# Kernel tuning notes

Measured on AMD Instinct MI355X. Metric: run time of the kernel, lower is better.

## Reference

```python
import jax, jax.numpy as jnp
import numpy as np

D = 256
H = 4
HD = D // H


def setup_inputs() -> dict:
    key = jax.random.key(0)
    ks = jax.random.split(key, 12)
    A, T = 64, 512
    s = 1.0 / np.sqrt(D)
    return {
        "features": jax.random.normal(ks[0], (A, T, D), jnp.float32),
        "positions": jax.random.normal(ks[1], (A, T, 2), jnp.float32),
        "Wq": jax.random.normal(ks[2], (D, D), jnp.float32) * s,
        "bq": jnp.zeros((D,), jnp.float32),
        "Wk": jax.random.normal(ks[3], (D, D), jnp.float32) * s,
        "bk": jnp.zeros((D,), jnp.float32),
        "Wv": jax.random.normal(ks[4], (D, D), jnp.float32) * s,
        "bv": jnp.zeros((D,), jnp.float32),
        "Wo": jax.random.normal(ks[5], (D, D), jnp.float32) * s,
        "bo": jnp.zeros((D,), jnp.float32),
        "max_distance": 2,
        "time_window": 64,
    }


def _sparse_mask(positions, max_distance, time_window):
    # positions: [A, T, 2] -> allowed [A, T, T]
    A, T, _ = positions.shape
    diff = positions[:, :, None, :] - positions[:, None, :, :]  # [A,T,T,2]
    dist2 = jnp.sum(diff * diff, axis=-1)                       # [A,T,T]
    t = jnp.arange(T)
    tmask = jnp.abs(t[:, None] - t[None, :]) <= time_window      # [T,T]
    return (dist2 <= float(max_distance) ** 2) & tmask[None]     # [A,T,T]


def reference(features, positions, Wq, bq, Wk, bk, Wv, bv, Wo, bo,
              max_distance, time_window):
    A, T, Dm = features.shape
    allowed = _sparse_mask(positions, max_distance, time_window)  # [A,T,T]
    q = features @ Wq.T + bq
    k = features @ Wk.T + bk
    v = features @ Wv.T + bv
    # split heads: [A, T, H, HD]
    q = q.reshape(A, T, H, HD)
    k = k.reshape(A, T, H, HD)
    v = v.reshape(A, T, H, HD)
    scale = 1.0 / np.sqrt(HD)
    scores = jnp.einsum("athd,ashd->ahts", q, k) * scale          # [A,H,T,T]
    scores = jnp.where(allowed[:, None], scores, -jnp.inf)
    attn = jax.nn.softmax(scores, axis=-1)
    out = jnp.einsum("ahts,ashd->athd", attn, v).reshape(A, T, Dm)
    return out @ Wo.T + bo
```

## Files before the change

### kernel.cpp

```cpp
#include <hip/hip_runtime.h>
#include <hip/hip_bf16.h>
#include <cstdint>
#include <cstddef>

typedef __attribute__((ext_vector_type(8))) _Float16 half8;
typedef __attribute__((ext_vector_type(4))) float floatx4;

#define MFMA16(a, b, c) __builtin_amdgcn_mfma_f32_16x16x32_f16((a), (b), (c), 0, 0, 0)

#define GLOAD_LDS16(g, l)                                                     \
    __builtin_amdgcn_global_load_lds(                                         \
        (const __attribute__((address_space(1))) void*)(g),                   \
        (__attribute__((address_space(3))) void*)(l), 16, 0, 0)

#define NFEAT 8388608

__device__ __forceinline__ void stage_dma(
    const _Float16* __restrict__ src, _Float16* __restrict__ lds,
    int wid, int lane)
{
#pragma unroll
    for (int i = 0; i < 4; ++i) {
        int grp = wid * 4 + i;
        int row = grp * 8 + (lane >> 3);
        int sc  = (lane & 7) ^ (row & 7);
        GLOAD_LDS16(src + (size_t)row * 256 + sc * 8, lds + grp * 512);
    }
}

__device__ __forceinline__ void stage_f32_s(
    const float* __restrict__ src, _Float16* __restrict__ lds, int tid,
    int dst_stride)
{
#pragma unroll
    for (int i = 0; i < 4; ++i) {
        int g   = tid + 256 * i;
        int row = g >> 3, chd = g & 7;
        int chs = chd ^ (row & 7);
        const float* s = src + (size_t)row * 256 + chs * 8;
        float4 v0 = *(const float4*)s;
        float4 v1 = *(const float4*)(s + 4);
        half8 h = { (_Float16)v0.x, (_Float16)v0.y, (_Float16)v0.z, (_Float16)v0.w,
                    (_Float16)v1.x, (_Float16)v1.y, (_Float16)v1.z, (_Float16)v1.w };
        *(half8*)(&lds[row * dst_stride + chd * 8]) = h;
    }
}

__global__ __launch_bounds__(256) void qkv_fused(
    const float* __restrict__ feat,
    const float* __restrict__ Wq, const float* __restrict__ Wk,
    const float* __restrict__ Wv,
    const float* __restrict__ bq, const float* __restrict__ bk,
    const float* __restrict__ bv,
    _Float16* __restrict__ Qb, _Float16* __restrict__ Kb, _Float16* __restrict__ Vb)
{
    __shared__ _Float16 Xs[128 * 256];
    __shared__ _Float16 Ws[128 * 64];

    const int n   = blockIdx.x;
    const int idx = n >> 3;
    const int bm  = (n & 7) * 32 + (idx >> 1);
    const int bn  = idx & 1;

    const int tid  = threadIdx.x;
    const int lane = tid & 63, wid = tid >> 6;
    const int quad = lane >> 4, l16 = lane & 15;
    const int wm = wid & 1, wn = wid >> 1;

    const float* Xg = feat + (size_t)bm * 128 * 256;
#pragma unroll
    for (int slab = 0; slab < 4; ++slab)
        stage_f32_s(Xg + slab * 64, Xs + slab * 64, tid, 256);
    __syncthreads();

#pragma unroll 1
    for (int z = 0; z < 3; ++z) {
        const float* W    = (z == 0) ? Wq : (z == 1) ? Wk : Wv;
        const float* bias = (z == 0) ? bq : (z == 1) ? bk : bv;
        _Float16*    outp = (z == 0) ? Qb : (z == 1) ? Kb : Vb;
        const float* Wg = W + (size_t)bn * 128 * 256;

        floatx4 acc[4][4] = {};
#pragma unroll 1
        for (int ks = 0; ks < 4; ++ks) {
            stage_f32_s(Wg + ks * 64, Ws, tid, 64);
            __syncthreads();
#pragma unroll
            for (int kh = 0; kh < 2; ++kh) {
                half8 af[4], bf[4];
#pragma unroll
                for (int mi = 0; mi < 4; ++mi) {
                    int row = wm * 64 + mi * 16 + l16;
                    int cs  = (kh * 4 + quad) ^ (row & 7);
                    af[mi] = *(const half8*)(&Xs[row * 256 + ks * 64 + cs * 8]);
                }
#pragma unroll
                for (int ni = 0; ni < 4; ++ni) {
                    int row = wn * 64 + ni * 16 + l16;
                    int cs  = (kh * 4 + quad) ^ (row & 7);
                    bf[ni] = *(const half8*)(&Ws[row * 64 + cs * 8]);
                }
#pragma unroll
                for (int mi = 0; mi < 4; ++mi)
#pragma unroll
                    for (int ni = 0; ni < 4; ++ni)
                        acc[mi][ni] = MFMA16(af[mi], bf[ni], acc[mi][ni]);
            }
            __syncthreads();
        }

#pragma unroll
        for (int ni = 0; ni < 4; ++ni) {
            int col = bn * 128 + wn * 64 + ni * 16 + l16;
            float bv2 = bias[col];
#pragma unroll
            for (int mi = 0; mi < 4; ++mi)
#pragma unroll
                for (int r = 0; r < 4; ++r) {
                    int row = bm * 128 + wm * 64 + mi * 16 + quad * 4 + r;
                    outp[(size_t)row * 256 + col] = (_Float16)(acc[mi][ni][r] + bv2);
                }
        }
    }
}

__global__ __launch_bounds__(256) void out_gemm(
    const _Float16* __restrict__ attnH, const float* __restrict__ Wo,
    const float* __restrict__ bo, float* __restrict__ out)
{
    __shared__ _Float16 As[128 * 64];
    __shared__ _Float16 Bs[128 * 64];

    const int n   = blockIdx.x;
    const int idx = n >> 3;
    const int bm  = (n & 7) * 32 + (idx >> 1);
    const int bn  = idx & 1;

    const int tid  = threadIdx.x;
    const int lane = tid & 63, wid = tid >> 6;
    const int quad = lane >> 4, l16 = lane & 15;
    const int wm = wid & 1, wn = wid >> 1;

    floatx4 acc[4][4] = {};
    const float* Wg = Wo + (size_t)bn * 128 * 256;

    for (int k0 = 0; k0 < 256; k0 += 64) {
        stage_dma(attnH + (size_t)bm * 128 * 256 + k0, As, wid, lane);
        stage_f32_s(Wg + k0, Bs, tid, 64);
        __syncthreads();
#pragma unroll
        for (int kh = 0; kh < 2; ++kh) {
            half8 af[4], bf[4];
#pragma unroll
            for (int mi = 0; mi < 4; ++mi) {
                int row = wm * 64 + mi * 16 + l16;
                int cs  = (kh * 4 + quad) ^ (row & 7);
                af[mi] = *(const half8*)(&As[row * 64 + cs * 8]);
            }
#pragma unroll
            for (int ni = 0; ni < 4; ++ni) {
                int row = wn * 64 + ni * 16 + l16;
                int cs  = (kh * 4 + quad) ^ (row & 7);
                bf[ni] = *(const half8*)(&Bs[row * 64 + cs * 8]);
            }
#pragma unroll
            for (int mi = 0; mi < 4; ++mi)
#pragma unroll
                for (int ni = 0; ni < 4; ++ni)
                    acc[mi][ni] = MFMA16(af[mi], bf[ni], acc[mi][ni]);
        }
        __syncthreads();
    }

#pragma unroll
    for (int ni = 0; ni < 4; ++ni) {
        int col = bn * 128 + wn * 64 + ni * 16 + l16;
        float bv = bo[col];
#pragma unroll
        for (int mi = 0; mi < 4; ++mi)
#pragma unroll
            for (int r = 0; r < 4; ++r) {
                int row = bm * 128 + wm * 64 + mi * 16 + quad * 4 + r;
                out[(size_t)row * 256 + col] = acc[mi][ni][r] + bv;
            }
    }
}

__global__ __launch_bounds__(256) void attn_kernel(
    const _Float16* __restrict__ Qb, const _Float16* __restrict__ Kb,
    const _Float16* __restrict__ Vb, const float* __restrict__ positions,
    const int* __restrict__ mdp, const int* __restrict__ twp,
    _Float16* __restrict__ attnb)
{
    const int n   = blockIdx.x;
    const int idx = n >> 3;
    const int a   = (n & 7) * 8 + (idx >> 5);
    const int rem = idx & 31;
    const int qt  = rem >> 2, h = rem & 3;

    const int q0 = qt * 64;
    const int s_base = q0 - 64;
    const int tid = threadIdx.x, lane = tid & 63, wid = tid >> 6;
    const int quad = lane >> 4, l16 = lane & 15;

    __shared__ _Float16 KPs[192 * 64];
    __shared__ _Float16 Vt[64 * 192];

    const size_t abase = (size_t)a * 512;
    const int md = *mdp, tw = *twp;
    const float md2 = (float)(md * md);

    const size_t qrow = abase + q0 + wid * 16 + l16;
    half8 aq0 = *(const half8*)(Qb + qrow * 256 + h * 64 + quad * 8);
    half8 aq1 = *(const half8*)(Qb + qrow * 256 + h * 64 + 32 + quad * 8);
    float qpx[4], qpy[4];
    int trow[4];
#pragma unroll
    for (int r = 0; r < 4; ++r) {
        int m = wid * 16 + quad * 4 + r;
        trow[r] = q0 + m;
        float2 qp = *(const float2*)(positions + (abase + q0 + m) * 2);
        qpx[r] = qp.x;
        qpy[r] = qp.y;
    }

#pragma unroll
    for (int i = 0; i < 6; ++i) {
        int grp = wid * 6 + i;
        int si  = grp * 8 + (lane >> 3);
        int sc  = min(max(s_base + si, 0), 511);
        int ch  = (lane & 7) ^ (si & 7);
        GLOAD_LDS16(Kb + (abase + sc) * 256 + h * 64 + ch * 8, KPs + grp * 512);
    }
#pragma unroll
    for (int i = 0; i < 3; ++i) {
        int g   = tid + 256 * i;
        int si2 = (g % 96) * 2;
        int d0  = (g / 96) * 8;
        int sa  = min(max(s_base + si2, 0), 511);
        int sb  = min(max(s_base + si2 + 1, 0), 511);
        half8 v0 = *(const half8*)(Vb + (abase + sa) * 256 + h * 64 + d0);
        half8 v1 = *(const half8*)(Vb + (abase + sb) * 256 + h * 64 + d0);
        int c = si2 >> 3;
#pragma unroll
        for (int j = 0; j < 8; ++j) {
            int d  = d0 + j;
            int cs = (c & ~7) | ((c & 7) ^ (d & 7));
            union { _Float16 hh[2]; uint32_t u; } p;
            p.hh[0] = v0[j]; p.hh[1] = v1[j];
            *(uint32_t*)(&Vt[d * 192 + cs * 8 + (si2 & 7)]) = p.u;
        }
    }
    __syncthreads();

    floatx4 S[12];
#pragma unroll
    for (int j = 0; j < 12; ++j) {
        int si = j * 16 + l16;
        half8 bk0 = *(const half8*)(&KPs[si * 64 + ((quad) ^ (si & 7)) * 8]);
        half8 bk1 = *(const half8*)(&KPs[si * 64 + ((4 + quad) ^ (si & 7)) * 8]);
        floatx4 acc = {};
        acc = MFMA16(aq0, bk0, acc);
        acc = MFMA16(aq1, bk1, acc);
        int sr = s_base + si;
        int sc = min(max(sr, 0), 511);
        float2 kp = *(const float2*)(positions + (abase + sc) * 2);
        bool svalid = (sr >= 0) && (sr < 512);
#pragma unroll
        for (int r = 0; r < 4; ++r) {
            float dx = qpx[r] - kp.x, dy = qpy[r] - kp.y;
            float d2 = dx * dx + dy * dy;
            int dt = trow[r] - sr; dt = dt < 0 ? -dt : dt;
            bool ok = svalid && (d2 <= md2) && (dt <= tw);
            S[j][r] = ok ? acc[r] * 0.125f : -1e30f;
        }
    }

    float minv[4];
#pragma unroll
    for (int r = 0; r < 4; ++r) {
        float m = -1e30f;
#pragma unroll
        for (int j = 0; j < 12; ++j) m = fmaxf(m, S[j][r]);
        m = fmaxf(m, __shfl_xor(m, 1));
        m = fmaxf(m, __shfl_xor(m, 2));
        m = fmaxf(m, __shfl_xor(m, 4));
        m = fmaxf(m, __shfl_xor(m, 8));
        float l = 0.f;
#pragma unroll
        for (int j = 0; j < 12; ++j) {
            float p = __expf(S[j][r] - m);
            S[j][r] = p;
            l += p;
        }
        l += __shfl_xor(l, 1);
        l += __shfl_xor(l, 2);
        l += __shfl_xor(l, 4);
        l += __shfl_xor(l, 8);
        minv[r] = 1.0f / l;
    }

    __syncthreads();

    _Float16* Ps = KPs + wid * (16 * 192);
#pragma unroll
    for (int j = 0; j < 12; ++j)
#pragma unroll
        for (int r = 0; r < 4; ++r) {
            int row = quad * 4 + r;
            int col = j * 16 + l16;
            int ch  = (col >> 3) ^ (row & 7);
            Ps[row * 192 + ch * 8 + (col & 7)] = (_Float16)(S[j][r] * minv[r]);
        }

    half8 af[6];
#pragma unroll
    for (int k = 0; k < 6; ++k) {
        int ch = (k * 4 + quad) ^ (l16 & 7);
        af[k] = *(const half8*)(&Ps[l16 * 192 + ch * 8]);
    }
#pragma unroll
    for (int nn = 0; nn < 4; ++nn) {
        floatx4 accO = {};
#pragma unroll
        for (int k = 0; k < 6; ++k) {
            int row = nn * 16 + l16;
            int c   = k * 4 + quad;
            int cs  = (c & ~7) | ((c & 7) ^ (row & 7));
            half8 bv = *(const half8*)(&Vt[row * 192 + cs * 8]);
            accO = MFMA16(af[k], bv, accO);
        }
#pragma unroll
        for (int r = 0; r < 4; ++r) {
            int row = q0 + wid * 16 + quad * 4 + r;
            attnb[(abase + row) * 256 + h * 64 + nn * 16 + l16] = (_Float16)accO[r];
        }
    }
}

extern "C" void kernel_launch(void* const* d_in, const int* in_sizes, int n_in,
                              void* d_out, int out_size, void* d_ws, size_t ws_size,
                              hipStream_t stream)
{
    const float* feat = (const float*)d_in[0];
    const float* pos  = (const float*)d_in[1];
    const float* Wq   = (const float*)d_in[2];
    const float* bq   = (const float*)d_in[3];
    const float* Wk   = (const float*)d_in[4];
    const float* bk   = (const float*)d_in[5];
    const float* Wv   = (const float*)d_in[6];
    const float* bv   = (const float*)d_in[7];
    const float* Wo   = (const float*)d_in[8];
    const float* bo   = (const float*)d_in[9];
    const int*   md   = (const int*)d_in[10];
    const int*   tw   = (const int*)d_in[11];
    float*       out  = (float*)d_out;

    _Float16* ws    = (_Float16*)d_ws;
    _Float16* Qb    = ws;
    _Float16* Kb    = Qb + NFEAT;
    _Float16* Vb    = Kb + NFEAT;
    _Float16* attnH = Vb + NFEAT;

    qkv_fused<<<512, 256, 0, stream>>>(feat, Wq, Wk, Wv, bq, bk, bv, Qb, Kb, Vb);

    attn_kernel<<<2048, 256, 0, stream>>>(Qb, Kb, Vb, pos, md, tw, attnH);

    out_gemm<<<512, 256, 0, stream>>>(attnH, Wo, bo, out);
}
```

Before: 166.2 us.

## Fuse attention and output projection into one kernel looping over heads

Merges the attention kernel and the output GEMM. Each block now handles one 64-query tile across all four heads, keeps the per-head outputs in LDS, then multiplies by Wo directly. This drops the fp16 attnH round trip through global memory and one kernel launch. In exchange the grid shrinks from 2048 to 512 blocks, heads run serially inside a block, LDS use grows to about 80KB, and every block re-stages all of Wo from fp32.

Measured after the change: 189.7 us. +14.2%, slower.

```diff
diff --git a/kernel.cpp b/kernel.cpp
--- a/kernel.cpp
+++ b/kernel.cpp
@@ -14,19 +14,6 @@
         (__attribute__((address_space(3))) void*)(l), 16, 0, 0)
 
 #define NFEAT 8388608
-
-__device__ __forceinline__ void stage_dma(
-    const _Float16* __restrict__ src, _Float16* __restrict__ lds,
-    int wid, int lane)
-{
-#pragma unroll
-    for (int i = 0; i < 4; ++i) {
-        int grp = wid * 4 + i;
-        int row = grp * 8 + (lane >> 3);
-        int sc  = (lane & 7) ^ (row & 7);
-        GLOAD_LDS16(src + (size_t)row * 256 + sc * 8, lds + grp * 512);
-    }
-}
 
 __device__ __forceinline__ void stage_f32_s(
     const float* __restrict__ src, _Float16* __restrict__ lds, int tid,
@@ -124,95 +111,33 @@
     }
 }
 
-__global__ __launch_bounds__(256) void out_gemm(
-    const _Float16* __restrict__ attnH, const float* __restrict__ Wo,
-    const float* __restrict__ bo, float* __restrict__ out)
-{
-    __shared__ _Float16 As[128 * 64];
-    __shared__ _Float16 Bs[128 * 64];
-
-    const int n   = blockIdx.x;
-    const int idx = n >> 3;
-    const int bm  = (n & 7) * 32 + (idx >> 1);
-    const int bn  = idx & 1;
-
-    const int tid  = threadIdx.x;
-    const int lane = tid & 63, wid = tid >> 6;
-    const int quad = lane >> 4, l16 = lane & 15;
-    const int wm = wid & 1, wn = wid >> 1;
-
-    floatx4 acc[4][4] = {};
-    const float* Wg = Wo + (size_t)bn * 128 * 256;
-
-    for (int k0 = 0; k0 < 256; k0 += 64) {
-        stage_dma(attnH + (size_t)bm * 128 * 256 + k0, As, wid, lane);
-        stage_f32_s(Wg + k0, Bs, tid, 64);
-        __syncthreads();
-#pragma unroll
-        for (int kh = 0; kh < 2; ++kh) {
-            half8 af[4], bf[4];
-#pragma unroll
-            for (int mi = 0; mi < 4; ++mi) {
-                int row = wm * 64 + mi * 16 + l16;
-                int cs  = (kh * 4 + quad) ^ (row & 7);
-                af[mi] = *(const half8*)(&As[row * 64 + cs * 8]);
-            }
-#pragma unroll
-            for (int ni = 0; ni < 4; ++ni) {
-                int row = wn * 64 + ni * 16 + l16;
-                int cs  = (kh * 4 + quad) ^ (row & 7);
-                bf[ni] = *(const half8*)(&Bs[row * 64 + cs * 8]);
-            }
-#pragma unroll
-            for (int mi = 0; mi < 4; ++mi)
-#pragma unroll
-                for (int ni = 0; ni < 4; ++ni)
-                    acc[mi][ni] = MFMA16(af[mi], bf[ni], acc[mi][ni]);
-        }
-        __syncthreads();
-    }
-
-#pragma unroll
-    for (int ni = 0; ni < 4; ++ni) {
-        int col = bn * 128 + wn * 64 + ni * 16 + l16;
-        float bv = bo[col];
-#pragma unroll
-        for (int mi = 0; mi < 4; ++mi)
-#pragma unroll
-            for (int r = 0; r < 4; ++r) {
-                int row = bm * 128 + wm * 64 + mi * 16 + quad * 4 + r;
-                out[(size_t)row * 256 + col] = acc[mi][ni][r] + bv;
-            }
-    }
-}
-
-__global__ __launch_bounds__(256) void attn_kernel(
+__global__ __launch_bounds__(256) void attn_out(
     const _Float16* __restrict__ Qb, const _Float16* __restrict__ Kb,
     const _Float16* __restrict__ Vb, const float* __restrict__ positions,
     const int* __restrict__ mdp, const int* __restrict__ twp,
-    _Float16* __restrict__ attnb)
+    const float* __restrict__ Wo, const float* __restrict__ bo,
+    float* __restrict__ out)
 {
+    __shared__ _Float16 KV[24576];
+    __shared__ _Float16 Os[64 * 256];
+
+    _Float16* KPs = KV;
+    _Float16* Vt  = KV + 12288;
+
     const int n   = blockIdx.x;
     const int idx = n >> 3;
-    const int a   = (n & 7) * 8 + (idx >> 5);
-    const int rem = idx & 31;
-    const int qt  = rem >> 2, h = rem & 3;
+    const int a   = (n & 7) * 8 + (idx >> 3);
+    const int qt  = idx & 7;
 
     const int q0 = qt * 64;
     const int s_base = q0 - 64;
     const int tid = threadIdx.x, lane = tid & 63, wid = tid >> 6;
     const int quad = lane >> 4, l16 = lane & 15;
 
-    __shared__ _Float16 KPs[192 * 64];
-    __shared__ _Float16 Vt[64 * 192];
-
     const size_t abase = (size_t)a * 512;
     const int md = *mdp, tw = *twp;
     const float md2 = (float)(md * md);
 
-    const size_t qrow = abase + q0 + wid * 16 + l16;
-    half8 aq0 = *(const half8*)(Qb + qrow * 256 + h * 64 + quad * 8);
-    half8 aq1 = *(const half8*)(Qb + qrow * 256 + h * 64 + 32 + quad * 8);
     float qpx[4], qpy[4];
     int trow[4];
 #pragma unroll
@@ -223,118 +148,172 @@
         qpx[r] = qp.x;
         qpy[r] = qp.y;
     }
-
-#pragma unroll
-    for (int i = 0; i < 6; ++i) {
-        int grp = wid * 6 + i;
-        int si  = grp * 8 + (lane >> 3);
-        int sc  = min(max(s_base + si, 0), 511);
-        int ch  = (lane & 7) ^ (si & 7);
-        GLOAD_LDS16(Kb + (abase + sc) * 256 + h * 64 + ch * 8, KPs + grp * 512);
-    }
-#pragma unroll
-    for (int i = 0; i < 3; ++i) {
-        int g   = tid + 256 * i;
-        int si2 = (g % 96) * 2;
-        int d0  = (g / 96) * 8;
-        int sa  = min(max(s_base + si2, 0), 511);
-        int sb  = min(max(s_base + si2 + 1, 0), 511);
-        half8 v0 = *(const half8*)(Vb + (abase + sa) * 256 + h * 64 + d0);
-        half8 v1 = *(const half8*)(Vb + (abase + sb) * 256 + h * 64 + d0);
-        int c = si2 >> 3;
-#pragma unroll
-        for (int j = 0; j < 8; ++j) {
-            int d  = d0 + j;
-            int cs = (c & ~7) | ((c & 7) ^ (d & 7));
-            union { _Float16 hh[2]; uint32_t u; } p;
-            p.hh[0] = v0[j]; p.hh[1] = v1[j];
-            *(uint32_t*)(&Vt[d * 192 + cs * 8 + (si2 & 7)]) = p.u;
-        }
-    }
-    __syncthreads();
-
-    floatx4 S[12];
-#pragma unroll
-    for (int j = 0; j < 12; ++j) {
-        int si = j * 16 + l16;
-        half8 bk0 = *(const half8*)(&KPs[si * 64 + ((quad) ^ (si & 7)) * 8]);
-        half8 bk1 = *(const half8*)(&KPs[si * 64 + ((4 + quad) ^ (si & 7)) * 8]);
-        floatx4 acc = {};
-        acc = MFMA16(aq0, bk0, acc);
-        acc = MFMA16(aq1, bk1, acc);
-        int sr = s_base + si;
-        int sc = min(max(sr, 0), 511);
-        float2 kp = *(const float2*)(positions + (abase + sc) * 2);
-        bool svalid = (sr >= 0) && (sr < 512);
+    const size_t qrow = abase + q0 + wid * 16 + l16;
+
+#pragma unroll 1
+    for (int h = 0; h < 4; ++h) {
+        half8 aq0 = *(const half8*)(Qb + qrow * 256 + h * 64 + quad * 8);
+        half8 aq1 = *(const half8*)(Qb + qrow * 256 + h * 64 + 32 + quad * 8);
+
+#pragma unroll
+        for (int i = 0; i < 6; ++i) {
+            int grp = wid * 6 + i;
+            int si  = grp * 8 + (lane >> 3);
+            int sc  = min(max(s_base + si, 0), 511);
+            int ch  = (lane & 7) ^ (si & 7);
+            GLOAD_LDS16(Kb + (abase + sc) * 256 + h * 64 + ch * 8, KPs + grp * 512);
+        }
+#pragma unroll
+        for (int i = 0; i < 3; ++i) {
+            int g   = tid + 256 * i;
+            int si2 = (g % 96) * 2;
+            int d0  = (g / 96) * 8;
+            int sa  = min(max(s_base + si2, 0), 511);
+            int sb  = min(max(s_base + si2 + 1, 0), 511);
+            half8 v0 = *(const half8*)(Vb + (abase + sa) * 256 + h * 64 + d0);
+            half8 v1 = *(const half8*)(Vb + (abase + sb) * 256 + h * 64 + d0);
+            int c = si2 >> 3;
+#pragma unroll
+            for (int j = 0; j < 8; ++j) {
+                int d  = d0 + j;
+                int cs = (c & ~7) | ((c & 7) ^ (d & 7));
+                union { _Float16 hh[2]; uint32_t u; } p;
+                p.hh[0] = v0[j]; p.hh[1] = v1[j];
+                *(uint32_t*)(&Vt[d * 192 + cs * 8 + (si2 & 7)]) = p.u;
+            }
+        }
+        __syncthreads();
+
+        floatx4 S[12];
+#pragma unroll
+        for (int j = 0; j < 12; ++j) {
+            int si = j * 16 + l16;
+            half8 bk0 = *(const half8*)(&KPs[si * 64 + ((quad) ^ (si & 7)) * 8]);
+            half8 bk1 = *(const half8*)(&KPs[si * 64 + ((4 + quad) ^ (si & 7)) * 8]);
+            floatx4 acc = {};
+            acc = MFMA16(aq0, bk0, acc);
+            acc = MFMA16(aq1, bk1, acc);
+            int sr = s_base + si;
+            int sc = min(max(sr, 0), 511);
+            float2 kp = *(const float2*)(positions + (abase + sc) * 2);
+            bool svalid = (sr >= 0) && (sr < 512);
+#pragma unroll
+            for (int r = 0; r < 4; ++r) {
+                float dx = qpx[r] - kp.x, dy = qpy[r] - kp.y;
+                float d2 = dx * dx + dy * dy;
+                int dt = trow[r] - sr; dt = dt < 0 ? -dt : dt;
+                bool ok = svalid && (d2 <= md2) && (dt <= tw);
+                S[j][r] = ok ? acc[r] * 0.125f : -1e30f;
+            }
+        }
+
+        float minv[4];
 #pragma unroll
         for (int r = 0; r < 4; ++r) {
-            float dx = qpx[r] - kp.x, dy = qpy[r] - kp.y;
-            float d2 = dx * dx + dy * dy;
-            int dt = trow[r] - sr; dt = dt < 0 ? -dt : dt;
-            bool ok = svalid && (d2 <= md2) && (dt <= tw);
-            S[j][r] = ok ? acc[r] * 0.125f : -1e30f;
-        }
-    }
-
-    float minv[4];
-#pragma unroll
-    for (int r = 0; r < 4; ++r) {
-        float m = -1e30f;
-#pragma unroll
-        for (int j = 0; j < 12; ++j) m = fmaxf(m, S[j][r]);
-        m = fmaxf(m, __shfl_xor(m, 1));
-        m = fmaxf(m, __shfl_xor(m, 2));
-        m = fmaxf(m, __shfl_xor(m, 4));
-        m = fmaxf(m, __shfl_xor(m, 8));
-        float l = 0.f;
-#pragma unroll
-        for (int j = 0; j < 12; ++j) {
-            float p = __expf(S[j][r] - m);
-            S[j][r] = p;
-            l += p;
-        }
-        l += __shfl_xor(l, 1);
-        l += __shfl_xor(l, 2);
-        l += __shfl_xor(l, 4);
-        l += __shfl_xor(l, 8);
-        minv[r] = 1.0f / l;
-    }
-
-    __syncthreads();
-
-    _Float16* Ps = KPs + wid * (16 * 192);
-#pragma unroll
-    for (int j = 0; j < 12; ++j)
-#pragma unroll
-        for (int r = 0; r < 4; ++r) {
-            int row = quad * 4 + r;
-            int col = j * 16 + l16;
-            int ch  = (col >> 3) ^ (row & 7);
-            Ps[row * 192 + ch * 8 + (col & 7)] = (_Float16)(S[j][r] * minv[r]);
-        }
-
-    half8 af[6];
-#pragma unroll
-    for (int k = 0; k < 6; ++k) {
-        int ch = (k * 4 + quad) ^ (l16 & 7);
-        af[k] = *(const half8*)(&Ps[l16 * 192 + ch * 8]);
-    }
-#pragma unroll
-    for (int nn = 0; nn < 4; ++nn) {
-        floatx4 accO = {};
+            float m = -1e30f;
+#pragma unroll
+            for (int j = 0; j < 12; ++j) m = fmaxf(m, S[j][r]);
+            m = fmaxf(m, __shfl_xor(m, 1));
+            m = fmaxf(m, __shfl_xor(m, 2));
+            m = fmaxf(m, __shfl_xor(m, 4));
+            m = fmaxf(m, __shfl_xor(m, 8));
+            float l = 0.f;
+#pragma unroll
+            for (int j = 0; j < 12; ++j) {
+                float p = __expf(S[j][r] - m);
+                S[j][r] = p;
+                l += p;
+            }
+            l += __shfl_xor(l, 1);
+            l += __shfl_xor(l, 2);
+            l += __shfl_xor(l, 4);
+            l += __shfl_xor(l, 8);
+            minv[r] = 1.0f / l;
+        }
+
+        __syncthreads();
+
+        _Float16* Ps = KPs + wid * (16 * 192);
+#pragma unroll
+        for (int j = 0; j < 12; ++j)
+#pragma unroll
+            for (int r = 0; r < 4; ++r) {
+                int row = quad * 4 + r;
+                int col = j * 16 + l16;
+                int ch  = (col >> 3) ^ (row & 7);
+                Ps[row * 192 + ch * 8 + (col & 7)] = (_Float16)(S[j][r] * minv[r]);
+            }
+
+        half8 af[6];
 #pragma unroll
         for (int k = 0; k < 6; ++k) {
-            int row = nn * 16 + l16;
-            int c   = k * 4 + quad;
-            int cs  = (c & ~7) | ((c & 7) ^ (row & 7));
-            half8 bv = *(const half8*)(&Vt[row * 192 + cs * 8]);
-            accO = MFMA16(af[k], bv, accO);
-        }
-#pragma unroll
-        for (int r = 0; r < 4; ++r) {
-            int row = q0 + wid * 16 + quad * 4 + r;
-            attnb[(abase + row) * 256 + h * 64 + nn * 16 + l16] = (_Float16)accO[r];
-        }
+            int ch = (k * 4 + quad) ^ (l16 & 7);
+            af[k] = *(const half8*)(&Ps[l16 * 192 + ch * 8]);
+        }
+#pragma unroll
+        for (int nn = 0; nn < 4; ++nn) {
+            floatx4 accO = {};
+#pragma unroll
+            for (int k = 0; k < 6; ++k) {
+                int row = nn * 16 + l16;
+                int c   = k * 4 + quad;
+                int cs  = (c & ~7) | ((c & 7) ^ (row & 7));
+                half8 bv = *(const half8*)(&Vt[row * 192 + cs * 8]);
+                accO = MFMA16(af[k], bv, accO);
+            }
+#pragma unroll
+            for (int r = 0; r < 4; ++r) {
+                int orow = wid * 16 + quad * 4 + r;
+                int c    = nn * 2 + (l16 >> 3);
+                int cs   = c ^ (orow & 7);
+                Os[orow * 256 + h * 64 + cs * 8 + (l16 & 7)] = (_Float16)accO[r];
+            }
+        }
+        __syncthreads();
+    }
+
+    _Float16* Wos = KV;
+    floatx4 acc[4][4] = {};
+#pragma unroll 1
+    for (int ks = 0; ks < 4; ++ks) {
+        stage_f32_s(Wo + ks * 64, Wos, tid, 64);
+        stage_f32_s(Wo + (size_t)128 * 256 + ks * 64, Wos + 128 * 64, tid, 64);
+        __syncthreads();
+#pragma unroll
+        for (int kh = 0; kh < 2; ++kh) {
+            half8 af2[4], bf[4];
+#pragma unroll
+            for (int mi = 0; mi < 4; ++mi) {
+                int row = mi * 16 + l16;
+                int cs  = (kh * 4 + quad) ^ (row & 7);
+                af2[mi] = *(const half8*)(&Os[row * 256 + ks * 64 + cs * 8]);
+            }
+#pragma unroll
+            for (int ni = 0; ni < 4; ++ni) {
+                int row = wid * 64 + ni * 16 + l16;
+                int cs  = (kh * 4 + quad) ^ (row & 7);
+                bf[ni] = *(const half8*)(&Wos[row * 64 + cs * 8]);
+            }
+#pragma unroll
+            for (int mi = 0; mi < 4; ++mi)
+#pragma unroll
+                for (int ni = 0; ni < 4; ++ni)
+                    acc[mi][ni] = MFMA16(af2[mi], bf[ni], acc[mi][ni]);
+        }
+        __syncthreads();
+    }
+
+#pragma unroll
+    for (int ni = 0; ni < 4; ++ni) {
+        int col = wid * 64 + ni * 16 + l16;
+        float bv2 = bo[col];
+#pragma unroll
+        for (int mi = 0; mi < 4; ++mi)
+#pragma unroll
+            for (int r = 0; r < 4; ++r) {
+                int row = q0 + mi * 16 + quad * 4 + r;
+                out[(abase + row) * 256 + col] = acc[mi][ni][r] + bv2;
+            }
     }
 }
 
@@ -356,15 +335,12 @@
     const int*   tw   = (const int*)d_in[11];
     float*       out  = (float*)d_out;
 
-    _Float16* ws    = (_Float16*)d_ws;
-    _Float16* Qb    = ws;
-    _Float16* Kb    = Qb + NFEAT;
-    _Float16* Vb    = Kb + NFEAT;
-    _Float16* attnH = Vb + NFEAT;
+    _Float16* ws = (_Float16*)d_ws;
+    _Float16* Qb = ws;
+    _Float16* Kb = Qb + NFEAT;
+    _Float16* Vb = Kb + NFEAT;
 
     qkv_fused<<<512, 256, 0, stream>>>(feat, Wq, Wk, Wv, bq, bk, bv, Qb, Kb, Vb);
 
-    attn_kernel<<<2048, 256, 0, stream>>>(Qb, Kb, Vb, pos, md, tw, attnH);
-
-    out_gemm<<<512, 256, 0, stream>>>(attnH, Wo, bo, out);
+    attn_out<<<512, 256, 0, stream>>>(Qb, Kb, Vb, pos, md, tw, Wo, bo, out);
 }
```

## Pre-convert features and weights to fp16, use async LDS DMA in GEMMs

Applied to the files above, without the earlier changes.

Adds a prep kernel that converts the fp32 features and all four weight matrices to fp16 in workspace. The QKV and output GEMMs then stage their tiles with direct global-to-LDS loads instead of per-thread fp32 loads, conversion and LDS stores. The X tile is re-laid out as four 64-column slabs to match the DMA staging. This adds an extra kernel launch and an extra full pass over the features (read fp32, write fp16, read fp16 again), trading that traffic for cheaper staging inside the GEMMs.

After: 185.6 us. +11.7%, slower.

```diff
diff --git a/kernel.cpp b/kernel.cpp
--- a/kernel.cpp
+++ b/kernel.cpp
@@ -14,6 +14,7 @@
         (__attribute__((address_space(3))) void*)(l), 16, 0, 0)
 
 #define NFEAT 8388608
+#define WELEM 65536
 
 __device__ __forceinline__ void stage_dma(
     const _Float16* __restrict__ src, _Float16* __restrict__ lds,
@@ -28,28 +29,47 @@
     }
 }
 
-__device__ __forceinline__ void stage_f32_s(
-    const float* __restrict__ src, _Float16* __restrict__ lds, int tid,
-    int dst_stride)
-{
-#pragma unroll
-    for (int i = 0; i < 4; ++i) {
-        int g   = tid + 256 * i;
-        int row = g >> 3, chd = g & 7;
-        int chs = chd ^ (row & 7);
-        const float* s = src + (size_t)row * 256 + chs * 8;
-        float4 v0 = *(const float4*)s;
-        float4 v1 = *(const float4*)(s + 4);
-        half8 h = { (_Float16)v0.x, (_Float16)v0.y, (_Float16)v0.z, (_Float16)v0.w,
-                    (_Float16)v1.x, (_Float16)v1.y, (_Float16)v1.z, (_Float16)v1.w };
-        *(half8*)(&lds[row * dst_stride + chd * 8]) = h;
+__device__ __forceinline__ half8 cvt8(const float* __restrict__ s)
+{
+    float4 v0 = *(const float4*)s;
+    float4 v1 = *(const float4*)(s + 4);
+    half8 h = { (_Float16)v0.x, (_Float16)v0.y, (_Float16)v0.z, (_Float16)v0.w,
+                (_Float16)v1.x, (_Float16)v1.y, (_Float16)v1.z, (_Float16)v1.w };
+    return h;
+}
+
+__global__ __launch_bounds__(256) void prep_cvt(
+    const float* __restrict__ feat, const float* __restrict__ Wq,
+    const float* __restrict__ Wk, const float* __restrict__ Wv,
+    const float* __restrict__ Wo,
+    _Float16* __restrict__ feath, _Float16* __restrict__ Wqh,
+    _Float16* __restrict__ Wkh, _Float16* __restrict__ Wvh,
+    _Float16* __restrict__ Woh)
+{
+    const int n = blockIdx.x, tid = threadIdx.x;
+    if (n < 2048) {
+#pragma unroll
+        for (int i = 0; i < 2; ++i) {
+            size_t idx = (size_t)n * 4096 + i * 2048 + tid * 8;
+            *(half8*)(feath + idx) = cvt8(feat + idx);
+        }
+    } else {
+        int m = n - 2048;
+        int w = m >> 3, blk = m & 7;
+        const float* src = (w == 0) ? Wq : (w == 1) ? Wk : (w == 2) ? Wv : Wo;
+        _Float16*    dst = (w == 0) ? Wqh : (w == 1) ? Wkh : (w == 2) ? Wvh : Woh;
+#pragma unroll
+        for (int i = 0; i < 4; ++i) {
+            size_t idx = (size_t)blk * 8192 + i * 2048 + tid * 8;
+            *(half8*)(dst + idx) = cvt8(src + idx);
+        }
     }
 }
 
 __global__ __launch_bounds__(256) void qkv_fused(
-    const float* __restrict__ feat,
-    const float* __restrict__ Wq, const float* __restrict__ Wk,
-    const float* __restrict__ Wv,
+    const _Float16* __restrict__ feath,
+    const _Float16* __restrict__ Wqh, const _Float16* __restrict__ Wkh,
+    const _Float16* __restrict__ Wvh,
     const float* __restrict__ bq, const float* __restrict__ bk,
     const float* __restrict__ bv,
     _Float16* __restrict__ Qb, _Float16* __restrict__ Kb, _Float16* __restrict__ Vb)
@@ -67,23 +87,23 @@
     const int quad = lane >> 4, l16 = lane & 15;
     const int wm = wid & 1, wn = wid >> 1;
 
-    const float* Xg = feat + (size_t)bm * 128 * 256;
+    const _Float16* Xg = feath + (size_t)bm * 128 * 256;
 #pragma unroll
     for (int slab = 0; slab < 4; ++slab)
-        stage_f32_s(Xg + slab * 64, Xs + slab * 64, tid, 256);
+        stage_dma(Xg + slab * 64, Xs + slab * 8192, wid, lane);
     __syncthreads();
 
 #pragma unroll 1
     for (int z = 0; z < 3; ++z) {
-        const float* W    = (z == 0) ? Wq : (z == 1) ? Wk : Wv;
-        const float* bias = (z == 0) ? bq : (z == 1) ? bk : bv;
-        _Float16*    outp = (z == 0) ? Qb : (z == 1) ? Kb : Vb;
-        const float* Wg = W + (size_t)bn * 128 * 256;
+        const _Float16* W  = (z == 0) ? Wqh : (z == 1) ? Wkh : Wvh;
+        const float* bias  = (z == 0) ? bq : (z == 1) ? bk : bv;
+        _Float16*    outp  = (z == 0) ? Qb : (z == 1) ? Kb : Vb;
+        const _Float16* Wg = W + (size_t)bn * 128 * 256;
 
         floatx4 acc[4][4] = {};
 #pragma unroll 1
         for (int ks = 0; ks < 4; ++ks) {
-            stage_f32_s(Wg + ks * 64, Ws, tid, 64);
+            stage_dma(Wg + ks * 64, Ws, wid, lane);
             __syncthreads();
 #pragma unroll
             for (int kh = 0; kh < 2; ++kh) {
@@ -92,7 +112,7 @@
                 for (int mi = 0; mi < 4; ++mi) {
                     int row = wm * 64 + mi * 16 + l16;
                     int cs  = (kh * 4 + quad) ^ (row & 7);
-                    af[mi] = *(const half8*)(&Xs[row * 256 + ks * 64 + cs * 8]);
+                    af[mi] = *(const half8*)(&Xs[ks * 8192 + row * 64 + cs * 8]);
                 }
 #pragma unroll
                 for (int ni = 0; ni < 4; ++ni) {
@@ -125,7 +145,7 @@
 }
 
 __global__ __launch_bounds__(256) void out_gemm(
-    const _Float16* __restrict__ attnH, const float* __restrict__ Wo,
+    const _Float16* __restrict__ attnH, const _Float16* __restrict__ Woh,
     const float* __restrict__ bo, float* __restrict__ out)
 {
     __shared__ _Float16 As[128 * 64];
@@ -142,11 +162,11 @@
     const int wm = wid & 1, wn = wid >> 1;
 
     floatx4 acc[4][4] = {};
-    const float* Wg = Wo + (size_t)bn * 128 * 256;
+    const _Float16* Wg = Woh + (size_t)bn * 128 * 256;
 
     for (int k0 = 0; k0 < 256; k0 += 64) {
         stage_dma(attnH + (size_t)bm * 128 * 256 + k0, As, wid, lane);
-        stage_f32_s(Wg + k0, Bs, tid, 64);
+        stage_dma(Wg + k0, Bs, wid, lane);
         __syncthreads();
 #pragma unroll
         for (int kh = 0; kh < 2; ++kh) {
@@ -361,10 +381,19 @@
     _Float16* Kb    = Qb + NFEAT;
     _Float16* Vb    = Kb + NFEAT;
     _Float16* attnH = Vb + NFEAT;
-
-    qkv_fused<<<512, 256, 0, stream>>>(feat, Wq, Wk, Wv, bq, bk, bv, Qb, Kb, Vb);
+    _Float16* feath = attnH + NFEAT;
+    _Float16* Wqh   = feath + NFEAT;
+    _Float16* Wkh   = Wqh + WELEM;
+    _Float16* Wvh   = Wkh + WELEM;
+    _Float16* Woh   = Wvh + WELEM;
+
+    prep_cvt<<<2080, 256, 0, stream>>>(feat, Wq, Wk, Wv, Wo,
+                                       feath, Wqh, Wkh, Wvh, Woh);
+
+    qkv_fused<<<512, 256, 0, stream>>>(feath, Wqh, Wkh, Wvh, bq, bk, bv,
+                                       Qb, Kb, Vb);
 
     attn_kernel<<<2048, 256, 0, stream>>>(Qb, Kb, Vb, pos, md, tw, attnH);
 
-    out_gemm<<<512, 256, 0, stream>>>(attnH, Wo, bo, out);
-}
+    out_gemm<<<512, 256, 0, stream>>>(attnH, Woh, bo, out);
+}
```

## Pre-convert weights to fp16 and restructure projection GEMMs with 64-row tiles

Applied to the files above, without the earlier changes.

A small prep kernel converts all four weight matrices to fp16 once per call. The QKV and output GEMMs switch to 64-row tiles that cover the full 256 output columns. Weight fragments are read straight from global memory (L2-resident) into registers, which removes the per-k-step LDS staging and its barriers. Both kernels also get a launch-bounds occupancy hint, and the attention kernel wraps its MFMA sections in s_setprio. The cost is one extra launch and L2-bound weight reads.

Result: slower. 190.0 us (+14.3%).

```diff
diff --git a/kernel.cpp b/kernel.cpp
--- a/kernel.cpp
+++ b/kernel.cpp
@@ -14,174 +14,174 @@
         (__attribute__((address_space(3))) void*)(l), 16, 0, 0)
 
 #define NFEAT 8388608
-
-__device__ __forceinline__ void stage_dma(
-    const _Float16* __restrict__ src, _Float16* __restrict__ lds,
-    int wid, int lane)
-{
+#define WELEM 65536
+
+__device__ __forceinline__ half8 cvt8(const float* __restrict__ s)
+{
+    float4 v0 = *(const float4*)s;
+    float4 v1 = *(const float4*)(s + 4);
+    half8 h = { (_Float16)v0.x, (_Float16)v0.y, (_Float16)v0.z, (_Float16)v0.w,
+                (_Float16)v1.x, (_Float16)v1.y, (_Float16)v1.z, (_Float16)v1.w };
+    return h;
+}
+
+__global__ __launch_bounds__(256) void prep_w(
+    const float* __restrict__ Wq, const float* __restrict__ Wk,
+    const float* __restrict__ Wv, const float* __restrict__ Wo,
+    _Float16* __restrict__ Wcat, _Float16* __restrict__ Woh)
+{
+    const int m = blockIdx.x, tid = threadIdx.x;
+    const int w = m >> 3, blk = m & 7;
+    const float* src = (w == 0) ? Wq : (w == 1) ? Wk : (w == 2) ? Wv : Wo;
+    _Float16*    dst = (w < 3) ? (Wcat + w * WELEM) : Woh;
 #pragma unroll
     for (int i = 0; i < 4; ++i) {
-        int grp = wid * 4 + i;
-        int row = grp * 8 + (lane >> 3);
-        int sc  = (lane & 7) ^ (row & 7);
-        GLOAD_LDS16(src + (size_t)row * 256 + sc * 8, lds + grp * 512);
-    }
-}
-
-__device__ __forceinline__ void stage_f32_s(
-    const float* __restrict__ src, _Float16* __restrict__ lds, int tid,
-    int dst_stride)
-{
-#pragma unroll
-    for (int i = 0; i < 4; ++i) {
-        int g   = tid + 256 * i;
-        int row = g >> 3, chd = g & 7;
-        int chs = chd ^ (row & 7);
-        const float* s = src + (size_t)row * 256 + chs * 8;
-        float4 v0 = *(const float4*)s;
-        float4 v1 = *(const float4*)(s + 4);
-        half8 h = { (_Float16)v0.x, (_Float16)v0.y, (_Float16)v0.z, (_Float16)v0.w,
-                    (_Float16)v1.x, (_Float16)v1.y, (_Float16)v1.z, (_Float16)v1.w };
-        *(half8*)(&lds[row * dst_stride + chd * 8]) = h;
-    }
-}
-
-__global__ __launch_bounds__(256) void qkv_fused(
-    const float* __restrict__ feat,
-    const float* __restrict__ Wq, const float* __restrict__ Wk,
-    const float* __restrict__ Wv,
+        size_t idx = (size_t)blk * 8192 + i * 2048 + tid * 8;
+        *(half8*)(dst + idx) = cvt8(src + idx);
+    }
+}
+
+__global__ __launch_bounds__(256, 2) void qkv_fused(
+    const float* __restrict__ feat, const _Float16* __restrict__ Wcat,
     const float* __restrict__ bq, const float* __restrict__ bk,
     const float* __restrict__ bv,
     _Float16* __restrict__ Qb, _Float16* __restrict__ Kb, _Float16* __restrict__ Vb)
 {
-    __shared__ _Float16 Xs[128 * 256];
-    __shared__ _Float16 Ws[128 * 64];
-
-    const int n   = blockIdx.x;
-    const int idx = n >> 3;
-    const int bm  = (n & 7) * 32 + (idx >> 1);
-    const int bn  = idx & 1;
+    __shared__ _Float16 Xs[64 * 256];
+
+    const int n  = blockIdx.x;
+    const int bm = (n & 7) * 64 + (n >> 3);
 
     const int tid  = threadIdx.x;
     const int lane = tid & 63, wid = tid >> 6;
     const int quad = lane >> 4, l16 = lane & 15;
-    const int wm = wid & 1, wn = wid >> 1;
-
-    const float* Xg = feat + (size_t)bm * 128 * 256;
-#pragma unroll
-    for (int slab = 0; slab < 4; ++slab)
-        stage_f32_s(Xg + slab * 64, Xs + slab * 64, tid, 256);
+
+    const float* Xg = feat + (size_t)bm * 64 * 256;
+#pragma unroll
+    for (int i = 0; i < 8; ++i) {
+        int g    = tid + 256 * i;
+        int row  = g >> 5, cg = g & 31;
+        int slab = cg >> 3, chd = cg & 7;
+        int chs  = chd ^ (row & 7);
+        *(half8*)(&Xs[slab * 4096 + row * 64 + chd * 8]) =
+            cvt8(Xg + row * 256 + slab * 64 + chs * 8);
+    }
     __syncthreads();
 
 #pragma unroll 1
     for (int z = 0; z < 3; ++z) {
-        const float* W    = (z == 0) ? Wq : (z == 1) ? Wk : Wv;
-        const float* bias = (z == 0) ? bq : (z == 1) ? bk : bv;
-        _Float16*    outp = (z == 0) ? Qb : (z == 1) ? Kb : Vb;
-        const float* Wg = W + (size_t)bn * 128 * 256;
+        const _Float16* Wz  = Wcat + z * WELEM;
+        const float* bias   = (z == 0) ? bq : (z == 1) ? bk : bv;
+        _Float16*    outp   = (z == 0) ? Qb : (z == 1) ? Kb : Vb;
 
         floatx4 acc[4][4] = {};
-#pragma unroll 1
+#pragma unroll
         for (int ks = 0; ks < 4; ++ks) {
-            stage_f32_s(Wg + ks * 64, Ws, tid, 64);
-            __syncthreads();
+            half8 bf[2][4];
+#pragma unroll
+            for (int kh = 0; kh < 2; ++kh)
+#pragma unroll
+                for (int ni = 0; ni < 4; ++ni) {
+                    int col = wid * 64 + ni * 16 + l16;
+                    bf[kh][ni] = *(const half8*)(
+                        Wz + (size_t)col * 256 + ks * 64 + kh * 32 + quad * 8);
+                }
 #pragma unroll
             for (int kh = 0; kh < 2; ++kh) {
-                half8 af[4], bf[4];
+                half8 af[4];
 #pragma unroll
                 for (int mi = 0; mi < 4; ++mi) {
-                    int row = wm * 64 + mi * 16 + l16;
+                    int row = mi * 16 + l16;
                     int cs  = (kh * 4 + quad) ^ (row & 7);
-                    af[mi] = *(const half8*)(&Xs[row * 256 + ks * 64 + cs * 8]);
+                    af[mi] = *(const half8*)(&Xs[ks * 4096 + row * 64 + cs * 8]);
                 }
 #pragma unroll
-                for (int ni = 0; ni < 4; ++ni) {
-                    int row = wn * 64 + ni * 16 + l16;
-                    int cs  = (kh * 4 + quad) ^ (row & 7);
-                    bf[ni] = *(const half8*)(&Ws[row * 64 + cs * 8]);
-                }
-#pragma unroll
                 for (int mi = 0; mi < 4; ++mi)
 #pragma unroll
                     for (int ni = 0; ni < 4; ++ni)
-                        acc[mi][ni] = MFMA16(af[mi], bf[ni], acc[mi][ni]);
+                        acc[mi][ni] = MFMA16(af[mi], bf[kh][ni], acc[mi][ni]);
             }
-            __syncthreads();
         }
 
 #pragma unroll
         for (int ni = 0; ni < 4; ++ni) {
-            int col = bn * 128 + wn * 64 + ni * 16 + l16;
+            int col = wid * 64 + ni * 16 + l16;
             float bv2 = bias[col];
 #pragma unroll
             for (int mi = 0; mi < 4; ++mi)
 #pragma unroll
                 for (int r = 0; r < 4; ++r) {
-                    int row = bm * 128 + wm * 64 + mi * 16 + quad * 4 + r;
+                    int row = bm * 64 + mi * 16 + quad * 4 + r;
                     outp[(size_t)row * 256 + col] = (_Float16)(acc[mi][ni][r] + bv2);
                 }
         }
     }
 }
 
-__global__ __launch_bounds__(256) void out_gemm(
-    const _Float16* __restrict__ attnH, const float* __restrict__ Wo,
+__global__ __launch_bounds__(256, 2) void out_gemm(
+    const _Float16* __restrict__ attnH, const _Float16* __restrict__ Woh,
     const float* __restrict__ bo, float* __restrict__ out)
 {
-    __shared__ _Float16 As[128 * 64];
-    __shared__ _Float16 Bs[128 * 64];
-
-    const int n   = blockIdx.x;
-    const int idx = n >> 3;
-    const int bm  = (n & 7) * 32 + (idx >> 1);
-    const int bn  = idx & 1;
+    __shared__ _Float16 As[64 * 256];
+
+    const int n  = blockIdx.x;
+    const int bm = (n & 7) * 64 + (n >> 3);
 
     const int tid  = threadIdx.x;
     const int lane = tid & 63, wid = tid >> 6;
     const int quad = lane >> 4, l16 = lane & 15;
-    const int wm = wid & 1, wn = wid >> 1;
+
+#pragma unroll
+    for (int slab = 0; slab < 4; ++slab)
+#pragma unroll
+        for (int i = 0; i < 2; ++i) {
+            int grp = wid * 2 + i;
+            int row = grp * 8 + (lane >> 3);
+            int sc  = (lane & 7) ^ (row & 7);
+            GLOAD_LDS16(attnH + ((size_t)(bm * 64 + row)) * 256 + slab * 64 + sc * 8,
+                        As + slab * 4096 + grp * 512);
+        }
+    __syncthreads();
 
     floatx4 acc[4][4] = {};
-    const float* Wg = Wo + (size_t)bn * 128 * 256;
-
-    for (int k0 = 0; k0 < 256; k0 += 64) {
-        stage_dma(attnH + (size_t)bm * 128 * 256 + k0, As, wid, lane);
-        stage_f32_s(Wg + k0, Bs, tid, 64);
-        __syncthreads();
+#pragma unroll
+    for (int ks = 0; ks < 4; ++ks) {
+        half8 bf[2][4];
+#pragma unroll
+        for (int kh = 0; kh < 2; ++kh)
+#pragma unroll
+            for (int ni = 0; ni < 4; ++ni) {
+                int col = wid * 64 + ni * 16 + l16;
+                bf[kh][ni] = *(const half8*)(
+                    Woh + (size_t)col * 256 + ks * 64 + kh * 32 + quad * 8);
+            }
 #pragma unroll
         for (int kh = 0; kh < 2; ++kh) {
-            half8 af[4], bf[4];
+            half8 af[4];
 #pragma unroll
             for (int mi = 0; mi < 4; ++mi) {
-                int row = wm * 64 + mi * 16 + l16;
+                int row = mi * 16 + l16;
                 int cs  = (kh * 4 + quad) ^ (row & 7);
-                af[mi] = *(const half8*)(&As[row * 64 + cs * 8]);
+                af[mi] = *(const half8*)(&As[ks * 4096 + row * 64 + cs * 8]);
             }
 #pragma unroll
-            for (int ni = 0; ni < 4; ++ni) {
-                int row = wn * 64 + ni * 16 + l16;
-                int cs  = (kh * 4 + quad) ^ (row & 7);
-                bf[ni] = *(const half8*)(&Bs[row * 64 + cs * 8]);
-            }
-#pragma unroll
             for (int mi = 0; mi < 4; ++mi)
 #pragma unroll
                 for (int ni = 0; ni < 4; ++ni)
-                    acc[mi][ni] = MFMA16(af[mi], bf[ni], acc[mi][ni]);
-        }
-        __syncthreads();
+                    acc[mi][ni] = MFMA16(af[mi], bf[kh][ni], acc[mi][ni]);
+        }
     }
 
 #pragma unroll
     for (int ni = 0; ni < 4; ++ni) {
-        int col = bn * 128 + wn * 64 + ni * 16 + l16;
-        float bv = bo[col];
+        int col = wid * 64 + ni * 16 + l16;
+        float bv2 = bo[col];
 #pragma unroll
         for (int mi = 0; mi < 4; ++mi)
 #pragma unroll
             for (int r = 0; r < 4; ++r) {
-                int row = bm * 128 + wm * 64 + mi * 16 + quad * 4 + r;
-                out[(size_t)row * 256 + col] = acc[mi][ni][r] + bv;
+                int row = bm * 64 + mi * 16 + quad * 4 + r;
+                out[(size_t)row * 256 + col] = acc[mi][ni][r] + bv2;
             }
     }
 }
@@ -260,8 +260,10 @@
         half8 bk0 = *(const half8*)(&KPs[si * 64 + ((quad) ^ (si & 7)) * 8]);
         half8 bk1 = *(const half8*)(&KPs[si * 64 + ((4 + quad) ^ (si & 7)) * 8]);
         floatx4 acc = {};
+        __builtin_amdgcn_s_setprio(1);
         acc = MFMA16(aq0, bk0, acc);
         acc = MFMA16(aq1, bk1, acc);
+        __builtin_amdgcn_s_setprio(0);
         int sr = s_base + si;
         int sc = min(max(sr, 0), 511);
         float2 kp = *(const float2*)(positions + (abase + sc) * 2);
@@ -322,6 +324,7 @@
 #pragma unroll
     for (int nn = 0; nn < 4; ++nn) {
         floatx4 accO = {};
+        __builtin_amdgcn_s_setprio(1);
 #pragma unroll
         for (int k = 0; k < 6; ++k) {
             int row = nn * 16 + l16;
@@ -330,6 +333,7 @@
             half8 bv = *(const half8*)(&Vt[row * 192 + cs * 8]);
             accO = MFMA16(af[k], bv, accO);
         }
+        __builtin_amdgcn_s_setprio(0);
 #pragma unroll
         for (int r = 0; r < 4; ++r) {
             int row = q0 + wid * 16 + quad * 4 + r;
@@ -361,10 +365,14 @@
     _Float16* Kb    = Qb + NFEAT;
     _Float16* Vb    = Kb + NFEAT;
     _Float16* attnH = Vb + NFEAT;
-
-    qkv_fused<<<512, 256, 0, stream>>>(feat, Wq, Wk, Wv, bq, bk, bv, Qb, Kb, Vb);
+    _Float16* Wcat  = attnH + NFEAT;
+    _Float16* Woh   = Wcat + 3 * WELEM;
+
+    prep_w<<<32, 256, 0, stream>>>(Wq, Wk, Wv, Wo, Wcat, Woh);
+
+    qkv_fused<<<512, 256, 0, stream>>>(feat, Wcat, bq, bk, bv, Qb, Kb, Vb);
 
     attn_kernel<<<2048, 256, 0, stream>>>(Qb, Kb, Vb, pos, md, tw, attnH);
 
-    out_gemm<<<512, 256, 0, stream>>>(attnH, Wo, bo, out);
-}
+    out_gemm<<<512, 256, 0, stream>>>(attnH, Woh, bo, out);
+}
```
